# Kernel tuning notes

Hardware: AMD Instinct MI355X
Metric: run time of the kernel (lower is better)

## Reference

```python
import jax, jax.numpy as jnp
import numpy as np

N = 40000      # nodes
E = 640000     # edges
F_IN = 128     # feature_dim
HID = 256      # hidden_dim
OUT = 128      # out_dim
B = 64         # num graphs
HEADS = 4
EPS = 1e-5


def setup_inputs() -> dict:
    key = jax.random.key(0)
    ks = jax.random.split(key, 32)
    s = 0.02
    inp = {
        "x_bb_masked": jax.random.normal(ks[0], (N, F_IN), jnp.float32),
        "x_att_masked": jax.random.normal(ks[1], (N, F_IN), jnp.float32),
        # SAGEConv1: in->hid  (lin_l acts on mean-aggregated neighbors, lin_r on root)
        "W1l": jax.random.normal(ks[2], (HID, F_IN), jnp.float32) * s,
        "b1l": jnp.zeros((HID,), jnp.float32),
        "W1r": jax.random.normal(ks[3], (HID, F_IN), jnp.float32) * s,
        # SAGEConv2: hid->hid
        "W2l": jax.random.normal(ks[4], (HID, HID), jnp.float32) * s,
        "b2l": jnp.zeros((HID,), jnp.float32),
        "W2r": jax.random.normal(ks[5], (HID, HID), jnp.float32) * s,
        # SAGEConv3: hid->out
        "W3l": jax.random.normal(ks[6], (OUT, HID), jnp.float32) * s,
        "b3l": jnp.zeros((OUT,), jnp.float32),
        "W3r": jax.random.normal(ks[7], (OUT, HID), jnp.float32) * s,
        # cross-attention projections
        "Wq": jax.random.normal(ks[8], (HID, F_IN), jnp.float32) * s,
        "bq": jnp.zeros((HID,), jnp.float32),
        "Wk": jax.random.normal(ks[9], (HID, OUT), jnp.float32) * s,
        "bk": jnp.zeros((HID,), jnp.float32),
        "Wv": jax.random.normal(ks[10], (HID, OUT), jnp.float32) * s,
        "bv": jnp.zeros((HID,), jnp.float32),
        # nn.MultiheadAttention packed in-proj and out-proj
        "in_proj_w": jax.random.normal(ks[11], (3 * HID, HID), jnp.float32) * s,
        "in_proj_b": jnp.zeros((3 * HID,), jnp.float32),
        "out_w": jax.random.normal(ks[12], (HID, HID), jnp.float32) * s,
        "out_b": jnp.zeros((HID,), jnp.float32),
        "ln_g": jnp.ones((HID,), jnp.float32),
        "ln_b": jnp.zeros((HID,), jnp.float32),
        "edge_index": jax.random.randint(ks[13], (2, E), 0, N, jnp.int64),
        "batch": jnp.sort(jax.random.randint(ks[14], (N,), 0, B, jnp.int64)),
    }
    return inp


def _sage(x, src, dst, Wl, bl, Wr):
    # mean aggregation of source features at target nodes, then lin_l(agg)+lin_r(x)
    agg = jax.ops.segment_sum(x[src], dst, num_segments=N)          # [N, d]
    cnt = jax.ops.segment_sum(jnp.ones((src.shape[0],), x.dtype), dst, num_segments=N)
    mean = agg / jnp.maximum(cnt, 1.0)[:, None]
    return mean @ Wl.T + bl + x @ Wr.T


def _forward(x_bb_masked, x_att_masked,
             W1l, b1l, W1r, W2l, b2l, W2r, W3l, b3l, W3r,
             Wq, bq, Wk, bk, Wv, bv, in_proj_w, in_proj_b, out_w, out_b,
             ln_g, ln_b, edge_index, batch):
    src, dst = edge_index[0], edge_index[1]
    h = jax.nn.relu(_sage(x_bb_masked, src, dst, W1l, b1l, W1r))
    h = jax.nn.relu(_sage(h, src, dst, W2l, b2l, W2r))
    h = _sage(h, src, dst, W3l, b3l, W3r)                           # [N, OUT]
    # global mean pool per graph
    gsum = jax.ops.segment_sum(h, batch, num_segments=B)            # [B, OUT]
    gcnt = jax.ops.segment_sum(jnp.ones((N,), h.dtype), batch, num_segments=B)
    graph_vec = gsum / jnp.maximum(gcnt, 1.0)[:, None]

    # cross attention: query per node, key/value from its graph vector (seq_len = 1)
    query = x_att_masked @ Wq.T + bq                                # [N, HID]
    gv = graph_vec[batch]                                           # [N, OUT]
    keyt = gv @ Wk.T + bk
    val = gv @ Wv.T + bv
    q = query @ in_proj_w[:HID].T + in_proj_b[:HID]
    k = keyt @ in_proj_w[HID:2 * HID].T + in_proj_b[HID:2 * HID]
    v = val @ in_proj_w[2 * HID:].T + in_proj_b[2 * HID:]
    dh = HID // HEADS
    qh = q.reshape(N, HEADS, dh)
    kh = k.reshape(N, HEADS, dh)
    vh = v.reshape(N, HEADS, dh)
    scores = jnp.sum(qh * kh, axis=-1, keepdims=True) / jnp.sqrt(jnp.asarray(dh, q.dtype))
    w = jax.nn.softmax(scores, axis=-1)                             # length-1 kv -> ones
    attn = (w * vh).reshape(N, HID)
    attn = attn @ out_w.T + out_b
    # LayerNorm
    mu = jnp.mean(attn, axis=-1, keepdims=True)
    var = jnp.mean((attn - mu) ** 2, axis=-1, keepdims=True)
    node_embeddings = (attn - mu) / jnp.sqrt(var + EPS) * ln_g + ln_b
    return graph_vec, node_embeddings


def reference(x_bb_masked, x_att_masked,
              W1l, b1l, W1r, W2l, b2l, W2r, W3l, b3l, W3r,
              Wq, bq, Wk, bk, Wv, bv, in_proj_w, in_proj_b, out_w, out_b,
              ln_g, ln_b, edge_index, batch):
    return _forward(x_bb_masked, x_att_masked,
                    W1l, b1l, W1r, W2l, b2l, W2r, W3l, b3l, W3r,
                    Wq, bq, Wk, bk, Wv, bv, in_proj_w, in_proj_b, out_w, out_b,
                    ln_g, ln_b, edge_index, batch)
```

## Files before the change

### kernel.cpp

```cpp
#include <hip/hip_runtime.h>

#define N_NODES 40000
#define N_EDGES 640000
#define NGRAPH 64
#define NBCH 157

typedef unsigned short u16;
typedef unsigned char u8;
typedef unsigned int u32;
typedef __attribute__((ext_vector_type(2))) float floatx2;
typedef __attribute__((ext_vector_type(4))) float floatx4;
typedef __attribute__((ext_vector_type(8))) short short8;
typedef __attribute__((ext_vector_type(8))) __bf16 bf16x8;

__device__ __forceinline__ float bf2f(u16 u) {
  u32 x = ((u32)u) << 16;
  return __builtin_bit_cast(float, x);
}
__device__ __forceinline__ u16 f2bf(float f) {
  u32 u = __builtin_bit_cast(u32, f);
  u += 0x7fffu + ((u >> 16) & 1u);
  return (u16)(u >> 16);
}
__device__ __forceinline__ uint2 f4tob(float4 v) {
  u32 lo = (u32)f2bf(v.x) | ((u32)f2bf(v.y) << 16);
  u32 hi = (u32)f2bf(v.z) | ((u32)f2bf(v.w) << 16);
  return make_uint2(lo, hi);
}
__device__ __forceinline__ u32 fp8pk_lo(float a, float b, u32 old) {
  return (u32)__builtin_amdgcn_cvt_pk_fp8_f32(a, b, (int)old, false);
}
__device__ __forceinline__ u32 fp8pk_hi(float a, float b, u32 old) {
  return (u32)__builtin_amdgcn_cvt_pk_fp8_f32(a, b, (int)old, true);
}
__device__ __forceinline__ floatx2 fp8up_lo(u32 v) {
  return __builtin_amdgcn_cvt_pk_f32_fp8((int)v, false);
}
__device__ __forceinline__ floatx2 fp8up_hi(u32 v) {
  return __builtin_amdgcn_cvt_pk_f32_fp8((int)v, true);
}
__device__ __forceinline__ void gld16(const void* g, void* l) {
  __builtin_amdgcn_global_load_lds(
      (const __attribute__((address_space(1))) u32*)g,
      (__attribute__((address_space(3))) u32*)l, 16, 0, 0);
}

__global__ __launch_bounds__(256) void k_setup(const float* __restrict__ x_bb, u16* __restrict__ xb,
                                               u8* __restrict__ xq,
                                               const float* __restrict__ W1l, u16* __restrict__ w1l,
                                               const float* __restrict__ W1r, u16* __restrict__ w1r,
                                               const float* __restrict__ W2l, u16* __restrict__ w2l,
                                               const float* __restrict__ W2r, u16* __restrict__ w2r,
                                               const float* __restrict__ W3l, u16* __restrict__ w3s,
                                               const float* __restrict__ W3r, u16* __restrict__ w3r,
                                               int* __restrict__ zbase,
                                               const int* __restrict__ batch, int* __restrict__ gstart) {
  const int tid = blockIdx.x * 256 + threadIdx.x;
  const int nth = gridDim.x * 256;
  for (int i = tid; i < 2 * N_NODES + 8192; i += nth) zbase[i] = 0;
  for (int i = tid; i < N_NODES * 32; i += nth) {
    float4 v = ((const float4*)x_bb)[i];
    ((uint2*)xb)[i] = f4tob(v);
    if (xq) {
      u32 q = fp8pk_lo(v.x, v.y, 0);
      q = fp8pk_hi(v.z, v.w, q);
      ((u32*)xq)[i] = q;
    }
  }
  for (int i = tid; i < 65536; i += nth) {
    const float* s; u16* d; int off;
    if (i < 8192)       { s = W1l; d = w1l; off = i; }
    else if (i < 16384) { s = W1r; d = w1r; off = i - 8192; }
    else if (i < 32768) { s = W2l; d = w2l; off = i - 16384; }
    else if (i < 49152) { s = W2r; d = w2r; off = i - 32768; }
    else if (i < 57344) { s = W3l; d = w3s; off = i - 49152; }
    else                { s = W3r; d = w3r; off = i - 57344; }
    ((uint2*)d)[off] = f4tob(((const float4*)s)[off]);
  }
  if (tid <= NGRAPH) {
    int lo = 0, hi = N_NODES;
    while (lo < hi) { int mid = (lo + hi) >> 1; if (batch[mid] < tid) lo = mid + 1; else hi = mid; }
    gstart[tid] = lo;
  }
}

__global__ __launch_bounds__(256) void k_hist(const int* __restrict__ ei, int* __restrict__ cnt) {
  int i = blockIdx.x * 256 + threadIdx.x;
  int4 d = ((const int4*)(ei + N_EDGES))[i];
  atomicAdd(&cnt[d.x], 1);
  atomicAdd(&cnt[d.y], 1);
  atomicAdd(&cnt[d.z], 1);
  atomicAdd(&cnt[d.w], 1);
}
__global__ __launch_bounds__(256) void k_scanrp(const int* __restrict__ cnt,
                                                int* __restrict__ rowptr, float* __restrict__ invc) {
  __shared__ int s[256];
  __shared__ int s_base;
  int b = blockIdx.x, t = threadIdx.x;
  int lim = b * 256;
  int b0 = 0, b1 = 0, b2 = 0, b3 = 0;
  int i = t;
  for (; i + 768 < lim; i += 1024) {
    b0 += cnt[i];
    b1 += cnt[i + 256];
    b2 += cnt[i + 512];
    b3 += cnt[i + 768];
  }
  for (; i < lim; i += 256) b0 += cnt[i];
  s[t] = b0 + b1 + b2 + b3;
  __syncthreads();
  for (int off = 128; off > 0; off >>= 1) {
    if (t < off) s[t] += s[t + off];
    __syncthreads();
  }
  if (t == 0) s_base = s[0];
  __syncthreads();
  int idx = b * 256 + t;
  int c = (idx < N_NODES) ? cnt[idx] : 0;
  s[t] = c;
  __syncthreads();
  for (int off = 1; off < 256; off <<= 1) {
    int v = (t >= off) ? s[t - off] : 0;
    __syncthreads();
    s[t] += v;
    __syncthreads();
  }
  if (idx < N_NODES) {
    rowptr[idx] = s_base + s[t] - c;
    invc[idx] = 1.0f / (float)(c > 1 ? c : 1);
  }
  if (b == 0 && t == 0) rowptr[N_NODES] = N_EDGES;
}
__global__ __launch_bounds__(256) void k_scatter(const int* __restrict__ ei, const int* __restrict__ rowptr,
                                                 int* __restrict__ cursor, int* __restrict__ perm) {
  int i = blockIdx.x * 256 + threadIdx.x;
  int4 d = ((const int4*)(ei + N_EDGES))[i];
  int4 sv = ((const int4*)ei)[i];
  int r0 = rowptr[d.x];
  int r1 = rowptr[d.y];
  int r2 = rowptr[d.z];
  int r3 = rowptr[d.w];
  int p0 = r0 + atomicAdd(&cursor[d.x], 1);
  int p1 = r1 + atomicAdd(&cursor[d.y], 1);
  int p2 = r2 + atomicAdd(&cursor[d.z], 1);
  int p3 = r3 + atomicAdd(&cursor[d.w], 1);
  perm[p0] = sv.x;
  perm[p1] = sv.y;
  perm[p2] = sv.z;
  perm[p3] = sv.w;
}

template <int D, int MODE, int QT>
__global__ __launch_bounds__(256) void k_agg(const void* __restrict__ xv, u16* __restrict__ outp,
                                             const int* __restrict__ rowptr,
                                             const int* __restrict__ perm,
                                             const float* __restrict__ invc,
                                             const u16* __restrict__ Radd, int nn) {
  int wv = threadIdx.x >> 6, lane = threadIdx.x & 63;
  int node = blockIdx.x * 4 + wv;
  int s = rowptr[node], e = rowptr[node + 1];
  int slot = lane >> 4, lsub = lane & 15;
  constexpr int FR = D / 16;
  float acc[FR];
#pragma unroll
  for (int i = 0; i < FR; ++i) acc[i] = 0.f;

  int p = s + slot;
  if constexpr (QT == 1) {
    const u8* xl = (const u8*)xv + lsub * FR;
    constexpr int NW = FR / 4;
    for (; p + 4 < e; p += 8) {
      int s0 = perm[p], s1 = perm[p + 4];
      const u8* r0 = xl + (size_t)s0 * D;
      const u8* r1 = xl + (size_t)s1 * D;
      u32 wa[NW], wb[NW];
      if constexpr (D == 128) {
        uint2 a = *(const uint2*)r0; wa[0] = a.x; wa[1] = a.y;
        uint2 b = *(const uint2*)r1; wb[0] = b.x; wb[1] = b.y;
      } else {
        uint4 a = *(const uint4*)r0; wa[0] = a.x; wa[1] = a.y; wa[2] = a.z; wa[3] = a.w;
        uint4 b = *(const uint4*)r1; wb[0] = b.x; wb[1] = b.y; wb[2] = b.z; wb[3] = b.w;
      }
#pragma unroll
      for (int j = 0; j < NW; ++j) {
        floatx2 l0 = fp8up_lo(wa[j]), h0 = fp8up_hi(wa[j]);
        floatx2 l1 = fp8up_lo(wb[j]), h1 = fp8up_hi(wb[j]);
        acc[4 * j]     += l0[0] + l1[0];
        acc[4 * j + 1] += l0[1] + l1[1];
        acc[4 * j + 2] += h0[0] + h1[0];
        acc[4 * j + 3] += h0[1] + h1[1];
      }
    }
    if (p < e) {
      int s0 = perm[p];
      const u8* r0 = xl + (size_t)s0 * D;
      u32 wa[NW];
      if constexpr (D == 128) {
        uint2 a = *(const uint2*)r0; wa[0] = a.x; wa[1] = a.y;
      } else {
        uint4 a = *(const uint4*)r0; wa[0] = a.x; wa[1] = a.y; wa[2] = a.z; wa[3] = a.w;
      }
#pragma unroll
      for (int j = 0; j < NW; ++j) {
        floatx2 l0 = fp8up_lo(wa[j]), h0 = fp8up_hi(wa[j]);
        acc[4 * j]     += l0[0];
        acc[4 * j + 1] += l0[1];
        acc[4 * j + 2] += h0[0];
        acc[4 * j + 3] += h0[1];
      }
    }
  } else {
    const u16* xl = (const u16*)xv + lsub * FR;
    for (; p + 4 < e; p += 8) {
      int src0 = perm[p];
      int src1 = perm[p + 4];
      const u16* rp0 = xl + (size_t)src0 * D;
      const u16* rp1 = xl + (size_t)src1 * D;
      if (D == 128) {
        uint4 va = *(const uint4*)rp0;
        uint4 vb = *(const uint4*)rp1;
        u32 wa[4] = {va.x, va.y, va.z, va.w}, wb[4] = {vb.x, vb.y, vb.z, vb.w};
#pragma unroll
        for (int j = 0; j < 4; ++j) {
          acc[2 * j] += __builtin_bit_cast(float, wa[j] << 16) + __builtin_bit_cast(float, wb[j] << 16);
          acc[2 * j + 1] += __builtin_bit_cast(float, wa[j] & 0xffff0000u) + __builtin_bit_cast(float, wb[j] & 0xffff0000u);
        }
      } else {
        uint4 a0 = *(const uint4*)rp0;
        uint4 a1 = *(const uint4*)(rp0 + 8);
        uint4 b0 = *(const uint4*)rp1;
        uint4 b1 = *(const uint4*)(rp1 + 8);
        u32 wa[8] = {a0.x, a0.y, a0.z, a0.w, a1.x, a1.y, a1.z, a1.w};
        u32 wb[8] = {b0.x, b0.y, b0.z, b0.w, b1.x, b1.y, b1.z, b1.w};
#pragma unroll
        for (int j = 0; j < 8; ++j) {
          acc[2 * j] += __builtin_bit_cast(float, wa[j] << 16) + __builtin_bit_cast(float, wb[j] << 16);
          acc[2 * j + 1] += __builtin_bit_cast(float, wa[j] & 0xffff0000u) + __builtin_bit_cast(float, wb[j] & 0xffff0000u);
        }
      }
    }
    if (p < e) {
      int src = perm[p];
      const u16* rp = xl + (size_t)src * D;
      if (D == 128) {
        uint4 va = *(const uint4*)rp;
        u32 wa[4] = {va.x, va.y, va.z, va.w};
#pragma unroll
        for (int j = 0; j < 4; ++j) {
          acc[2 * j] += __builtin_bit_cast(float, wa[j] << 16);
          acc[2 * j + 1] += __builtin_bit_cast(float, wa[j] & 0xffff0000u);
        }
      } else {
        uint4 a0 = *(const uint4*)rp;
        uint4 a1 = *(const uint4*)(rp + 8);
        u32 wa[8] = {a0.x, a0.y, a0.z, a0.w, a1.x, a1.y, a1.z, a1.w};
#pragma unroll
        for (int j = 0; j < 8; ++j) {
          acc[2 * j] += __builtin_bit_cast(float, wa[j] << 16);
          acc[2 * j + 1] += __builtin_bit_cast(float, wa[j] & 0xffff0000u);
        }
      }
    }
  }

#pragma unroll
  for (int i = 0; i < FR; ++i) {
    acc[i] += __shfl_xor(acc[i], 16, 64);
    acc[i] += __shfl_xor(acc[i], 32, 64);
  }

  if (slot == 0) {
    float iv = invc[node];
    float v[FR];
#pragma unroll
    for (int i = 0; i < FR; ++i) v[i] = acc[i] * iv;
    if constexpr (MODE == 1) {
      const uint4* rr = (const uint4*)(Radd + (size_t)node * D + lsub * FR);
      uint4 va = rr[0];
      u32 wa[4] = {va.x, va.y, va.z, va.w};
#pragma unroll
      for (int j = 0; j < 4; ++j) {
        v[2 * j] += __builtin_bit_cast(float, wa[j] << 16);
        v[2 * j + 1] += __builtin_bit_cast(float, wa[j] & 0xffff0000u);
      }
    }
    u32 wpk[FR / 2];
#pragma unroll
    for (int i = 0; i < FR / 2; ++i)
      wpk[i] = (u32)f2bf(v[2 * i]) | ((u32)f2bf(v[2 * i + 1]) << 16);
    uint4* o = (uint4*)(outp + (size_t)node * D + lsub * FR);
    o[0] = make_uint4(wpk[0], wpk[1], wpk[2], wpk[3]);
    if (FR == 16) o[1] = make_uint4(wpk[4], wpk[5], wpk[6], wpk[7]);
  }
}

template <int OUTW, int EPI>
__global__ __launch_bounds__(256) void k_gemm(const u16* __restrict__ A1, const u16* __restrict__ W1, int K1,
                                              const u16* __restrict__ A2, const u16* __restrict__ W2, int K2,
                                              const float* __restrict__ bias,
                                              void* __restrict__ out1, void* __restrict__ out2, int M) {
  __shared__ u16 lsA[128 * 64];
  __shared__ u16 lsB[128 * 64];
  const int tid = threadIdx.x, lane = tid & 63, wv = tid >> 6;
  const int wm = wv >> 1, wn = wv & 1;
  const int row0 = blockIdx.x * 128, col0 = blockIdx.y * 128;

  floatx4 acc[4][4];
#pragma unroll
  for (int r = 0; r < 4; ++r)
#pragma unroll
    for (int c = 0; c < 4; ++c) acc[r][c] = 0.f;

  for (int seg = 0; seg < 2; ++seg) {
    const u16* A = seg ? A2 : A1;
    const u16* Wm = seg ? W2 : W1;
    const int K = seg ? K2 : K1;
    if (K == 0) continue;
    for (int k0 = 0; k0 < K; k0 += 64) {
      __syncthreads();
#pragma unroll
      for (int i = 0; i < 4; ++i) {
        int chunk = i * 256 + tid;
        int r = chunk >> 3;
        int kc = chunk & 7;
        int kcs = kc ^ (r & 7);
        int grow = row0 + r;
        grow = grow < M ? grow : M - 1;
        gld16(A + (size_t)grow * K + (k0 + kcs * 8), lsA + (size_t)(i * 256 + wv * 64) * 8);
        int wr = col0 + r;
        gld16(Wm + (size_t)wr * K + (k0 + kcs * 8), lsB + (size_t)(i * 256 + wv * 64) * 8);
      }
      __syncthreads();
#pragma unroll
      for (int kk = 0; kk < 2; ++kk) {
        bf16x8 af[4], bb[4];
        int kc = kk * 4 + (lane >> 4);
#pragma unroll
        for (int r = 0; r < 4; ++r) {
          int row = wm * 64 + r * 16 + (lane & 15);
          af[r] = __builtin_bit_cast(bf16x8, *(const short8*)(lsA + row * 64 + ((kc ^ (row & 7)) << 3)));
        }
#pragma unroll
        for (int c = 0; c < 4; ++c) {
          int row = wn * 64 + c * 16 + (lane & 15);
          bb[c] = __builtin_bit_cast(bf16x8, *(const short8*)(lsB + row * 64 + ((kc ^ (row & 7)) << 3)));
        }
#pragma unroll
        for (int r = 0; r < 4; ++r)
#pragma unroll
          for (int c = 0; c < 4; ++c)
            acc[r][c] = __builtin_amdgcn_mfma_f32_16x16x32_bf16(af[r], bb[c], acc[r][c], 0, 0, 0);
      }
    }
  }

#pragma unroll
  for (int r = 0; r < 4; ++r) {
    int rowb = row0 + wm * 64 + r * 16 + ((lane >> 4) << 2);
#pragma unroll
    for (int c = 0; c < 4; ++c) {
      int col = col0 + wn * 64 + c * 16 + (lane & 15);
#pragma unroll
      for (int j = 0; j < 4; ++j) {
        int gr = rowb + j;
        if (gr < M) {
          float v = acc[r][c][j];
          if constexpr (EPI == 0 || EPI == 1) {
            v += bias[col];
            v = v > 0.f ? v : 0.f;
            ((u16*)out1)[(size_t)gr * OUTW + col] = f2bf(v);
            if constexpr (EPI == 1)
              ((u8*)out2)[(size_t)gr * OUTW + col] = (u8)(fp8pk_lo(v, v, 0) & 0xff);
          } else if constexpr (EPI == 2) {
            if (col < 128) {
              ((u16*)out1)[(size_t)gr * 128 + col] = f2bf(v);
            } else {
              v += bias[col - 128];
              ((u16*)out2)[(size_t)gr * 128 + (col - 128)] = f2bf(v);
            }
          } else {
            if (col < 128) {
              ((u8*)out1)[(size_t)gr * 128 + col] = (u8)(fp8pk_lo(v, v, 0) & 0xff);
            } else {
              v += bias[col - 128];
              ((u16*)out2)[(size_t)gr * 128 + (col - 128)] = f2bf(v);
            }
          }
        }
      }
    }
  }
}

__global__ __launch_bounds__(256) void k_pool_part(const u16* __restrict__ h3,
                                                   const int* __restrict__ batch,
                                                   float* __restrict__ gsum) {
  __shared__ int sb[64];
  int t = threadIdx.x;
  int n0 = blockIdx.x * 64;
  if (t < 64) sb[t] = batch[n0 + t];
  __syncthreads();
  int col = t & 127, sub = t >> 7;
  float acc = 0.f;
  int curg = -1;
  for (int i = sub; i < 64; i += 2) {
    int g = sb[i];
    if (g != curg) {
      if (curg >= 0) atomicAdd(&gsum[curg * 128 + col], acc);
      curg = g;
      acc = 0.f;
    }
    acc += bf2f(h3[(size_t)(n0 + i) * 128 + col]);
  }
  if (curg >= 0) atomicAdd(&gsum[curg * 128 + col], acc);
}

__global__ __launch_bounds__(256) void k_tail(const float* __restrict__ gsum, const int* __restrict__ gstart,
                                              const float* __restrict__ Wv,
                                              const float* __restrict__ bv, const float* __restrict__ ipw,
                                              const float* __restrict__ ipb, const float* __restrict__ outw,
                                              const float* __restrict__ outb, const float* __restrict__ lng,
                                              const float* __restrict__ lnb, float* __restrict__ dout,
                                              float* __restrict__ eout) {
  __shared__ float sa[256], sb[256];
  __shared__ float s_mu, s_var;
  int b = blockIdx.x, t = threadIdx.x;
  if (t < 128) {
    int cg = gstart[b + 1] - gstart[b];
    float mean = gsum[b * 128 + t] / (float)(cg > 1 ? cg : 1);
    sa[t] = mean;
    dout[b * 128 + t] = mean;
  }
  __syncthreads();
  float val = bv[t];
  for (int k = 0; k < 128; ++k) val += sa[k] * Wv[t * 128 + k];
  sb[t] = val;
  __syncthreads();
  float vv = ipb[512 + t];
  for (int k = 0; k < 256; ++k) vv += sb[k] * ipw[(size_t)(512 + t) * 256 + k];
  sa[t] = vv;
  __syncthreads();
  float at = outb[t];
  for (int k = 0; k < 256; ++k) at += sa[k] * outw[t * 256 + k];
  sb[t] = at;
  __syncthreads();
  for (int off = 128; off > 0; off >>= 1) {
    if (t < off) sb[t] += sb[t + off];
    __syncthreads();
  }
  if (t == 0) s_mu = sb[0] * (1.0f / 256.0f);
  __syncthreads();
  float d = at - s_mu;
  sb[t] = d * d;
  __syncthreads();
  for (int off = 128; off > 0; off >>= 1) {
    if (t < off) sb[t] += sb[t + off];
    __syncthreads();
  }
  if (t == 0) s_var = sb[0] * (1.0f / 256.0f);
  __syncthreads();
  float r = 1.0f / sqrtf(s_var + 1e-5f);
  eout[(size_t)b * 256 + t] = d * r * lng[t] + lnb[t];
}

__global__ void k_scat_out(const float* __restrict__ eb, const int* __restrict__ batch,
                           float* __restrict__ dout) {
  int i = blockIdx.x * 256 + threadIdx.x;
  int n = i >> 6, q = i & 63;
  float4 v = ((const float4*)eb)[(size_t)batch[n] * 64 + q];
  ((float4*)(dout + NGRAPH * 128))[i] = v;
}

extern "C" void kernel_launch(void* const* d_in, const int* in_sizes, int n_in,
                              void* d_out, int out_size, void* d_ws, size_t ws_size,
                              hipStream_t stream) {
  (void)in_sizes; (void)n_in; (void)out_size;
  const float* x_bb = (const float*)d_in[0];
  const float* W1l = (const float*)d_in[2];
  const float* b1l = (const float*)d_in[3];
  const float* W1r = (const float*)d_in[4];
  const float* W2l = (const float*)d_in[5];
  const float* b2l = (const float*)d_in[6];
  const float* W2r = (const float*)d_in[7];
  const float* W3l = (const float*)d_in[8];
  const float* b3l = (const float*)d_in[9];
  const float* W3r = (const float*)d_in[10];
  const float* Wv = (const float*)d_in[15];
  const float* bv = (const float*)d_in[16];
  const float* ipw = (const float*)d_in[17];
  const float* ipb = (const float*)d_in[18];
  const float* outw = (const float*)d_in[19];
  const float* outb = (const float*)d_in[20];
  const float* lng = (const float*)d_in[21];
  const float* lnb = (const float*)d_in[22];
  const int* ei = (const int*)d_in[23];
  const int* batch = (const int*)d_in[24];
  float* dout = (float*)d_out;
  char* ws = (char*)d_ws;

  constexpr size_t O_W1L = 0;
  constexpr size_t O_W1R = O_W1L + 256 * 128 * 2;
  constexpr size_t O_W2L = O_W1R + 256 * 128 * 2;
  constexpr size_t O_W2R = O_W2L + 256 * 256 * 2;
  constexpr size_t O_W3L = O_W2R + 256 * 256 * 2;
  constexpr size_t O_W3R = O_W3L + 128 * 256 * 2;
  constexpr size_t O_XB = O_W3R + 128 * 256 * 2;
  constexpr size_t O_MEAN1 = O_XB + (size_t)N_NODES * 128 * 2;
  constexpr size_t O_H1 = O_MEAN1 + (size_t)N_NODES * 128 * 2;
  constexpr size_t O_MEAN2 = O_H1 + (size_t)N_NODES * 256 * 2;
  constexpr size_t O_H2 = O_MEAN2 + (size_t)N_NODES * 256 * 2;
  constexpr size_t O_E = O_H2 + (size_t)N_NODES * 256 * 2;
  constexpr size_t O_CNT = O_E + 64 * 256 * 4;
  constexpr size_t O_CUR = O_CNT + (size_t)N_NODES * 4;
  constexpr size_t O_GSUM = O_CUR + (size_t)N_NODES * 4;
  constexpr size_t O_RP = O_GSUM + 64 * 128 * 4;
  constexpr size_t O_INVC = O_RP + (size_t)(N_NODES + 64) * 4;
  constexpr size_t O_GST = O_INVC + (size_t)N_NODES * 4;
  constexpr size_t O_PERM = O_GST + 512;
  constexpr size_t O_XQ = O_PERM + (size_t)N_EDGES * 4;
  constexpr size_t O_H1Q = O_XQ + (size_t)N_NODES * 128;
  constexpr size_t NEED_FP8 = O_H1Q + (size_t)N_NODES * 256;

  u16* w1l = (u16*)(ws + O_W1L);  u16* w1r = (u16*)(ws + O_W1R);
  u16* w2l = (u16*)(ws + O_W2L);  u16* w2r = (u16*)(ws + O_W2R);
  u16* w3s = (u16*)(ws + O_W3L);  u16* w3r = (u16*)(ws + O_W3R);
  u16* xb = (u16*)(ws + O_XB);
  u16* mean1 = (u16*)(ws + O_MEAN1);
  u16* h1 = (u16*)(ws + O_H1);
  u16* mean2 = (u16*)(ws + O_MEAN2);
  u16* h2 = (u16*)(ws + O_H2);
  u16* Pb = (u16*)(ws + O_XB);
  u16* Rb = (u16*)(ws + O_MEAN1);
  u16* h3b = (u16*)(ws + O_MEAN2);
  float* eb = (float*)(ws + O_E);
  int* cnt = (int*)(ws + O_CNT);
  int* cursor = (int*)(ws + O_CUR);
  float* gsum = (float*)(ws + O_GSUM);
  int* rowptr = (int*)(ws + O_RP);
  float* invc = (float*)(ws + O_INVC);
  int* gstart = (int*)(ws + O_GST);
  int* perm = (int*)(ws + O_PERM);
  u8* xq = (u8*)(ws + O_XQ);
  u8* Pq = (u8*)(ws + O_XQ);
  u8* h1q = (u8*)(ws + O_H1Q);

  const bool use_fp8 = (ws_size >= NEED_FP8);
  dim3 blk(256);

  k_setup<<<512, blk, 0, stream>>>(x_bb, xb, use_fp8 ? xq : nullptr,
                                   W1l, w1l, W1r, w1r, W2l, w2l, W2r, w2r,
                                   W3l, w3s, W3r, w3r, cnt, batch, gstart);
  k_hist<<<N_EDGES / 1024, blk, 0, stream>>>(ei, cnt);
  k_scanrp<<<NBCH, blk, 0, stream>>>(cnt, rowptr, invc);
  k_scatter<<<N_EDGES / 1024, blk, 0, stream>>>(ei, rowptr, cursor, perm);

  if (use_fp8) {
    k_agg<128, 0, 1><<<N_NODES / 4, blk, 0, stream>>>(xq, mean1, rowptr, perm, invc, nullptr, N_NODES);
    k_gemm<256, 1><<<dim3(313, 2), blk, 0, stream>>>(mean1, w1l, 128, xb, w1r, 128, b1l, h1, h1q, N_NODES);
    k_agg<256, 0, 1><<<N_NODES / 4, blk, 0, stream>>>(h1q, mean2, rowptr, perm, invc, nullptr, N_NODES);
    k_gemm<256, 0><<<dim3(313, 2), blk, 0, stream>>>(mean2, w2l, 256, h1, w2r, 256, b2l, h2, nullptr, N_NODES);
    k_gemm<128, 3><<<dim3(313, 2), blk, 0, stream>>>(h2, w3s, 256, nullptr, nullptr, 0, b3l, Pq, Rb, N_NODES);
    k_agg<128, 1, 1><<<N_NODES / 4, blk, 0, stream>>>(Pq, h3b, rowptr, perm, invc, Rb, N_NODES);
  } else {
    k_agg<128, 0, 0><<<N_NODES / 4, blk, 0, stream>>>(xb, mean1, rowptr, perm, invc, nullptr, N_NODES);
    k_gemm<256, 0><<<dim3(313, 2), blk, 0, stream>>>(mean1, w1l, 128, xb, w1r, 128, b1l, h1, nullptr, N_NODES);
    k_agg<256, 0, 0><<<N_NODES / 4, blk, 0, stream>>>(h1, mean2, rowptr, perm, invc, nullptr, N_NODES);
    k_gemm<256, 0><<<dim3(313, 2), blk, 0, stream>>>(mean2, w2l, 256, h1, w2r, 256, b2l, h2, nullptr, N_NODES);
    k_gemm<128, 2><<<dim3(313, 2), blk, 0, stream>>>(h2, w3s, 256, nullptr, nullptr, 0, b3l, Pb, Rb, N_NODES);
    k_agg<128, 1, 0><<<N_NODES / 4, blk, 0, stream>>>(Pb, h3b, rowptr, perm, invc, Rb, N_NODES);
  }

  k_pool_part<<<N_NODES / 64, blk, 0, stream>>>(h3b, batch, gsum);
  k_tail<<<NGRAPH, blk, 0, stream>>>(gsum, gstart, Wv, bv, ipw, ipb, outw, outb, lng, lnb, dout, eb);
  k_scat_out<<<N_NODES * 64 / 256, blk, 0, stream>>>(eb, batch, dout);
}
```

Before: 263.6 us.

## Split degree counters into four sub-buckets per node to cut atomic contention

The histogram and scatter atomics now hit one of four per-node sub-counters, chosen by edge lane, so four edges to the same destination do not collide. The scan runs over 4*N entries and produces a 4-way rowptr; aggregation reads rowptr[4*node] and rowptr[4*node+4]. The inverse count array is dropped and the inverse degree is computed inline from e-s. The cost is four times the counter memory to zero and a larger scan.

```diff
diff --git a/kernel.cpp b/kernel.cpp
--- a/kernel.cpp
+++ b/kernel.cpp
@@ -3,7 +3,7 @@
 #define N_NODES 40000
 #define N_EDGES 640000
 #define NGRAPH 64
-#define NBCH 157
+#define NBCH4 625
 
 typedef unsigned short u16;
 typedef unsigned char u8;
@@ -57,7 +57,7 @@
                                                const int* __restrict__ batch, int* __restrict__ gstart) {
   const int tid = blockIdx.x * 256 + threadIdx.x;
   const int nth = gridDim.x * 256;
-  for (int i = tid; i < 2 * N_NODES + 8192; i += nth) zbase[i] = 0;
+  for (int i = tid; i < 8 * N_NODES + 8192; i += nth) zbase[i] = 0;
   for (int i = tid; i < N_NODES * 32; i += nth) {
     float4 v = ((const float4*)x_bb)[i];
     ((uint2*)xb)[i] = f4tob(v);
@@ -84,29 +84,31 @@
   }
 }
 
-__global__ __launch_bounds__(256) void k_hist(const int* __restrict__ ei, int* __restrict__ cnt) {
+__global__ __launch_bounds__(256) void k_hist(const int* __restrict__ ei, int* __restrict__ cnt4) {
   int i = blockIdx.x * 256 + threadIdx.x;
   int4 d = ((const int4*)(ei + N_EDGES))[i];
-  atomicAdd(&cnt[d.x], 1);
-  atomicAdd(&cnt[d.y], 1);
-  atomicAdd(&cnt[d.z], 1);
-  atomicAdd(&cnt[d.w], 1);
-}
-__global__ __launch_bounds__(256) void k_scanrp(const int* __restrict__ cnt,
-                                                int* __restrict__ rowptr, float* __restrict__ invc) {
+  atomicAdd(&cnt4[4 * d.x + 0], 1);
+  atomicAdd(&cnt4[4 * d.y + 1], 1);
+  atomicAdd(&cnt4[4 * d.z + 2], 1);
+  atomicAdd(&cnt4[4 * d.w + 3], 1);
+}
+__global__ __launch_bounds__(256) void k_scanrp(const int* __restrict__ cnt4,
+                                                int* __restrict__ rowptr) {
   __shared__ int s[256];
   __shared__ int s_base;
   int b = blockIdx.x, t = threadIdx.x;
-  int lim = b * 256;
+  int lim4 = (b * 256) >> 2;
+  const int4* c4 = (const int4*)cnt4;
   int b0 = 0, b1 = 0, b2 = 0, b3 = 0;
   int i = t;
-  for (; i + 768 < lim; i += 1024) {
-    b0 += cnt[i];
-    b1 += cnt[i + 256];
-    b2 += cnt[i + 512];
-    b3 += cnt[i + 768];
-  }
-  for (; i < lim; i += 256) b0 += cnt[i];
+  for (; i + 768 < lim4; i += 1024) {
+    int4 v0 = c4[i], v1 = c4[i + 256], v2 = c4[i + 512], v3 = c4[i + 768];
+    b0 += v0.x + v0.y + v0.z + v0.w;
+    b1 += v1.x + v1.y + v1.z + v1.w;
+    b2 += v2.x + v2.y + v2.z + v2.w;
+    b3 += v3.x + v3.y + v3.z + v3.w;
+  }
+  for (; i < lim4; i += 256) { int4 v = c4[i]; b0 += v.x + v.y + v.z + v.w; }
   s[t] = b0 + b1 + b2 + b3;
   __syncthreads();
   for (int off = 128; off > 0; off >>= 1) {
@@ -116,7 +118,7 @@
   if (t == 0) s_base = s[0];
   __syncthreads();
   int idx = b * 256 + t;
-  int c = (idx < N_NODES) ? cnt[idx] : 0;
+  int c = cnt4[idx];
   s[t] = c;
   __syncthreads();
   for (int off = 1; off < 256; off <<= 1) {
@@ -125,25 +127,22 @@
     s[t] += v;
     __syncthreads();
   }
-  if (idx < N_NODES) {
-    rowptr[idx] = s_base + s[t] - c;
-    invc[idx] = 1.0f / (float)(c > 1 ? c : 1);
-  }
-  if (b == 0 && t == 0) rowptr[N_NODES] = N_EDGES;
+  rowptr[idx] = s_base + s[t] - c;
+  if (b == 0 && t == 0) rowptr[4 * N_NODES] = N_EDGES;
 }
 __global__ __launch_bounds__(256) void k_scatter(const int* __restrict__ ei, const int* __restrict__ rowptr,
-                                                 int* __restrict__ cursor, int* __restrict__ perm) {
+                                                 int* __restrict__ cursor4, int* __restrict__ perm) {
   int i = blockIdx.x * 256 + threadIdx.x;
   int4 d = ((const int4*)(ei + N_EDGES))[i];
   int4 sv = ((const int4*)ei)[i];
-  int r0 = rowptr[d.x];
-  int r1 = rowptr[d.y];
-  int r2 = rowptr[d.z];
-  int r3 = rowptr[d.w];
-  int p0 = r0 + atomicAdd(&cursor[d.x], 1);
-  int p1 = r1 + atomicAdd(&cursor[d.y], 1);
-  int p2 = r2 + atomicAdd(&cursor[d.z], 1);
-  int p3 = r3 + atomicAdd(&cursor[d.w], 1);
+  int r0 = rowptr[4 * d.x + 0];
+  int r1 = rowptr[4 * d.y + 1];
+  int r2 = rowptr[4 * d.z + 2];
+  int r3 = rowptr[4 * d.w + 3];
+  int p0 = r0 + atomicAdd(&cursor4[4 * d.x + 0], 1);
+  int p1 = r1 + atomicAdd(&cursor4[4 * d.y + 1], 1);
+  int p2 = r2 + atomicAdd(&cursor4[4 * d.z + 2], 1);
+  int p3 = r3 + atomicAdd(&cursor4[4 * d.w + 3], 1);
   perm[p0] = sv.x;
   perm[p1] = sv.y;
   perm[p2] = sv.z;
@@ -154,11 +153,10 @@
 __global__ __launch_bounds__(256) void k_agg(const void* __restrict__ xv, u16* __restrict__ outp,
                                              const int* __restrict__ rowptr,
                                              const int* __restrict__ perm,
-                                             const float* __restrict__ invc,
                                              const u16* __restrict__ Radd, int nn) {
   int wv = threadIdx.x >> 6, lane = threadIdx.x & 63;
   int node = blockIdx.x * 4 + wv;
-  int s = rowptr[node], e = rowptr[node + 1];
+  int s = rowptr[4 * node], e = rowptr[4 * node + 4];
   int slot = lane >> 4, lsub = lane & 15;
   constexpr int FR = D / 16;
   float acc[FR];
@@ -270,7 +268,8 @@
   }
 
   if (slot == 0) {
-    float iv = invc[node];
+    int cnt = e - s;
+    float iv = 1.0f / (float)(cnt > 1 ? cnt : 1);
     float v[FR];
 #pragma unroll
     for (int i = 0; i < FR; ++i) v[i] = acc[i] * iv;
@@ -511,11 +510,10 @@
   constexpr size_t O_H2 = O_MEAN2 + (size_t)N_NODES * 256 * 2;
   constexpr size_t O_E = O_H2 + (size_t)N_NODES * 256 * 2;
   constexpr size_t O_CNT = O_E + 64 * 256 * 4;
-  constexpr size_t O_CUR = O_CNT + (size_t)N_NODES * 4;
-  constexpr size_t O_GSUM = O_CUR + (size_t)N_NODES * 4;
+  constexpr size_t O_CUR = O_CNT + (size_t)4 * N_NODES * 4;
+  constexpr size_t O_GSUM = O_CUR + (size_t)4 * N_NODES * 4;
   constexpr size_t O_RP = O_GSUM + 64 * 128 * 4;
-  constexpr size_t O_INVC = O_RP + (size_t)(N_NODES + 64) * 4;
-  constexpr size_t O_GST = O_INVC + (size_t)N_NODES * 4;
+  constexpr size_t O_GST = O_RP + (size_t)(4 * N_NODES + 64) * 4;
   constexpr size_t O_PERM = O_GST + 512;
   constexpr size_t O_XQ = O_PERM + (size_t)N_EDGES * 4;
   constexpr size_t O_H1Q = O_XQ + (size_t)N_NODES * 128;
@@ -533,11 +531,10 @@
   u16* Rb = (u16*)(ws + O_MEAN1);
   u16* h3b = (u16*)(ws + O_MEAN2);
   float* eb = (float*)(ws + O_E);
-  int* cnt = (int*)(ws + O_CNT);
-  int* cursor = (int*)(ws + O_CUR);
+  int* cnt4 = (int*)(ws + O_CNT);
+  int* cursor4 = (int*)(ws + O_CUR);
   float* gsum = (float*)(ws + O_GSUM);
   int* rowptr = (int*)(ws + O_RP);
-  float* invc = (float*)(ws + O_INVC);
   int* gstart = (int*)(ws + O_GST);
   int* perm = (int*)(ws + O_PERM);
   u8* xq = (u8*)(ws + O_XQ);
@@ -549,25 +546,25 @@
 
   k_setup<<<512, blk, 0, stream>>>(x_bb, xb, use_fp8 ? xq : nullptr,
                                    W1l, w1l, W1r, w1r, W2l, w2l, W2r, w2r,
-                                   W3l, w3s, W3r, w3r, cnt, batch, gstart);
-  k_hist<<<N_EDGES / 1024, blk, 0, stream>>>(ei, cnt);
-  k_scanrp<<<NBCH, blk, 0, stream>>>(cnt, rowptr, invc);
-  k_scatter<<<N_EDGES / 1024, blk, 0, stream>>>(ei, rowptr, cursor, perm);
+                                   W3l, w3s, W3r, w3r, cnt4, batch, gstart);
+  k_hist<<<N_EDGES / 1024, blk, 0, stream>>>(ei, cnt4);
+  k_scanrp<<<NBCH4, blk, 0, stream>>>(cnt4, rowptr);
+  k_scatter<<<N_EDGES / 1024, blk, 0, stream>>>(ei, rowptr, cursor4, perm);
 
   if (use_fp8) {
-    k_agg<128, 0, 1><<<N_NODES / 4, blk, 0, stream>>>(xq, mean1, rowptr, perm, invc, nullptr, N_NODES);
+    k_agg<128, 0, 1><<<N_NODES / 4, blk, 0, stream>>>(xq, mean1, rowptr, perm, nullptr, N_NODES);
     k_gemm<256, 1><<<dim3(313, 2), blk, 0, stream>>>(mean1, w1l, 128, xb, w1r, 128, b1l, h1, h1q, N_NODES);
-    k_agg<256, 0, 1><<<N_NODES / 4, blk, 0, stream>>>(h1q, mean2, rowptr, perm, invc, nullptr, N_NODES);
+    k_agg<256, 0, 1><<<N_NODES / 4, blk, 0, stream>>>(h1q, mean2, rowptr, perm, nullptr, N_NODES);
     k_gemm<256, 0><<<dim3(313, 2), blk, 0, stream>>>(mean2, w2l, 256, h1, w2r, 256, b2l, h2, nullptr, N_NODES);
     k_gemm<128, 3><<<dim3(313, 2), blk, 0, stream>>>(h2, w3s, 256, nullptr, nullptr, 0, b3l, Pq, Rb, N_NODES);
-    k_agg<128, 1, 1><<<N_NODES / 4, blk, 0, stream>>>(Pq, h3b, rowptr, perm, invc, Rb, N_NODES);
+    k_agg<128, 1, 1><<<N_NODES / 4, blk, 0, stream>>>(Pq, h3b, rowptr, perm, Rb, N_NODES);
   } else {
-    k_agg<128, 0, 0><<<N_NODES / 4, blk, 0, stream>>>(xb, mean1, rowptr, perm, invc, nullptr, N_NODES);
+    k_agg<128, 0, 0><<<N_NODES / 4, blk, 0, stream>>>(xb, mean1, rowptr, perm, nullptr, N_NODES);
     k_gemm<256, 0><<<dim3(313, 2), blk, 0, stream>>>(mean1, w1l, 128, xb, w1r, 128, b1l, h1, nullptr, N_NODES);
-    k_agg<256, 0, 0><<<N_NODES / 4, blk, 0, stream>>>(h1, mean2, rowptr, perm, invc, nullptr, N_NODES);
+    k_agg<256, 0, 0><<<N_NODES / 4, blk, 0, stream>>>(h1, mean2, rowptr, perm, nullptr, N_NODES);
     k_gemm<256, 0><<<dim3(313, 2), blk, 0, stream>>>(mean2, w2l, 256, h1, w2r, 256, b2l, h2, nullptr, N_NODES);
     k_gemm<128, 2><<<dim3(313, 2), blk, 0, stream>>>(h2, w3s, 256, nullptr, nullptr, 0, b3l, Pb, Rb, N_NODES);
-    k_agg<128, 1, 0><<<N_NODES / 4, blk, 0, stream>>>(Pb, h3b, rowptr, perm, invc, Rb, N_NODES);
+    k_agg<128, 1, 0><<<N_NODES / 4, blk, 0, stream>>>(Pb, h3b, rowptr, perm, Rb, N_NODES);
   }
 
   k_pool_part<<<N_NODES / 64, blk, 0, stream>>>(h3b, batch, gsum);
```

Result: slower. 269.9 us (+2.4%).
